# Kernel tuning notes

Hardware: AMD Instinct MI355X
Metric: run time of the kernel (lower is better)

The kernel has to match this reference:

```python
import jax, jax.numpy as jnp
import numpy as np

D_MODEL = 1024
D_STATE = 16
D_CONV = 4
EXPAND = 2
HEADDIM = 64
NGROUPS = 1
D_INNER = EXPAND * D_MODEL            # 2048
NHEADS = D_INNER // HEADDIM           # 32
CONV_DIM = D_INNER + 2 * NGROUPS * D_STATE   # 2080
D_IN_PROJ = 2 * D_INNER + 2 * NGROUPS * D_STATE + NHEADS  # 4160
EPS = 1e-5
BATCH, SEQLEN = 4, 2048


def setup_inputs() -> dict:
    key = jax.random.key(0)
    ks = jax.random.split(key, 8)
    x = jax.random.normal(ks[0], (BATCH, SEQLEN, D_MODEL), jnp.float32)
    W_in = jax.random.normal(ks[1], (D_MODEL, D_IN_PROJ), jnp.float32) * 0.02
    conv_w = jax.random.normal(ks[2], (CONV_DIM, D_CONV), jnp.float32) * 0.2
    conv_b = jnp.zeros((CONV_DIM,), jnp.float32)
    # dt_bias = inverse softplus of dt drawn in [1e-3, 1e-1] (mamba_ssm init)
    dt = jax.random.uniform(ks[3], (NHEADS,), jnp.float32, 0.001, 0.1)
    dt_bias = jnp.log(jnp.expm1(dt))
    A_log = jnp.log(jax.random.uniform(ks[4], (NHEADS,), jnp.float32, 1.0, 16.0))
    D_param = jnp.ones((NHEADS,), jnp.float32)
    norm_w = jnp.ones((D_INNER,), jnp.float32)
    W_out = jax.random.normal(ks[5], (D_INNER, D_MODEL), jnp.float32) * 0.02
    layer_scale = jnp.full((D_MODEL,), 1e-4, jnp.float32)
    return dict(x=x, W_in=W_in, conv_w=conv_w, conv_b=conv_b, dt_bias=dt_bias,
                A_log=A_log, D_param=D_param, norm_w=norm_w, W_out=W_out,
                layer_scale=layer_scale)


def _silu(v):
    return v * jax.nn.sigmoid(v)


def _mamba2(x, W_in, conv_w, conv_b, dt_bias, A_log, D_param, norm_w, W_out):
    b, l, _ = x.shape
    zxbcdt = x @ W_in                                  # (b, l, d_in_proj)
    z = zxbcdt[..., :D_INNER]                          # gate
    xBC = zxbcdt[..., D_INNER:D_INNER + CONV_DIM]
    dt = jax.nn.softplus(zxbcdt[..., D_INNER + CONV_DIM:] + dt_bias)  # (b, l, h)
    # causal depthwise conv1d (kernel D_CONV) + SiLU
    xp = jnp.pad(xBC, ((0, 0), (D_CONV - 1, 0), (0, 0)))
    conv = sum(xp[:, k:k + l, :] * conv_w[:, k] for k in range(D_CONV)) + conv_b
    xBC = _silu(conv)
    xs = xBC[..., :D_INNER].reshape(b, l, NHEADS, HEADDIM)  # (b, l, h, p)
    Bm = xBC[..., D_INNER:D_INNER + D_STATE]                # (b, l, n), ngroups=1
    Cm = xBC[..., D_INNER + D_STATE:]                       # (b, l, n)
    A = -jnp.exp(A_log)                                     # (h,)
    dA = jnp.exp(dt * A)                                    # (b, l, h)
    dtx = dt[..., None] * xs                                # (b, l, h, p)

    def step(h, inp):
        dA_t, dtx_t, B_t, C_t = inp
        # h: (b, h, p, n)
        h = h * dA_t[..., None, None] + dtx_t[..., None] * B_t[:, None, None, :]
        y = jnp.einsum('bhpn,bn->bhp', h, C_t)
        return h, y

    h0 = jnp.zeros((b, NHEADS, HEADDIM, D_STATE), x.dtype)
    _, ys = jax.lax.scan(step, h0, (dA.transpose(1, 0, 2), dtx.transpose(1, 0, 2, 3),
                                    Bm.transpose(1, 0, 2), Cm.transpose(1, 0, 2)))
    y = ys.transpose(1, 0, 2, 3) + D_param[None, None, :, None] * xs  # (b, l, h, p)
    y = y.reshape(b, l, D_INNER)
    # gated RMSNorm (norm_before_gate=False): gate first, then rmsnorm
    y = y * _silu(z)
    y = y * jax.lax.rsqrt(jnp.mean(y * y, axis=-1, keepdims=True) + EPS) * norm_w
    return y @ W_out


def reference(x, W_in, conv_w, conv_b, dt_bias, A_log, D_param, norm_w, W_out, layer_scale):
    # dropout is identity (eval / p=0)
    return x + _mamba2(x, W_in, conv_w, conv_b, dt_bias, A_log, D_param, norm_w, W_out) * layer_scale
```

## Files before the change

kernel.cpp:

```cpp
#include <hip/hip_runtime.h>
#include <hip/hip_bf16.h>

#define D_MODEL   1024
#define D_STATE   16
#define D_CONV    4
#define HEADDIM   64
#define NHEADS    32
#define D_INNER   2048
#define CONV_DIM  2080
#define D_IN_PROJ 4160
#define NPAD      4224
#define BATCH     4
#define SEQLEN    2048
#define MROWS     (BATCH*SEQLEN)
#define QCHUNK    64
#define NCHUNK    (SEQLEN/QCHUNK)
#define DT_COL    (2*D_INNER + 2*D_STATE)

#define WSCALE    16.f
#define YSCALE    64.f

__device__ __forceinline__ unsigned short f2b(float f) {
    union { float f; unsigned int u; } v; v.f = f;
    unsigned int r = (v.u + 0x7FFFu + ((v.u >> 16) & 1u)) >> 16;
    return (unsigned short)r;
}
__device__ __forceinline__ float b2f(unsigned short h) {
    union { unsigned int u; float f; } v; v.u = ((unsigned int)h) << 16;
    return v.f;
}
__device__ __forceinline__ unsigned char f2fp8(float f) {
    return (unsigned char)(__builtin_amdgcn_cvt_pk_fp8_f32(f, 0.f, 0, false) & 0xFF);
}

typedef __attribute__((ext_vector_type(8))) short bf16x8;
typedef __attribute__((ext_vector_type(4))) float f32x4;
typedef __attribute__((ext_vector_type(4))) int   i32x4;
typedef __attribute__((ext_vector_type(8))) int   i32x8;

__device__ __forceinline__ i32x8 cat8(i32x4 a, i32x4 b) {
    i32x8 r;
    r[0] = a[0]; r[1] = a[1]; r[2] = a[2]; r[3] = a[3];
    r[4] = b[0]; r[5] = b[1]; r[6] = b[2]; r[7] = b[3];
    return r;
}

__device__ __forceinline__ void async_copy16b(const unsigned char* g, unsigned char* l) {
    __builtin_amdgcn_global_load_lds(
        (const __attribute__((address_space(1))) void*)g,
        (__attribute__((address_space(3))) void*)l, 16, 0, 0);
}

__global__ __launch_bounds__(256)
void pre_kernel(const float* __restrict__ x, unsigned char* __restrict__ x_f8,
                const float* __restrict__ W_in, unsigned char* __restrict__ winT,
                const float* __restrict__ W_out, unsigned char* __restrict__ woutT,
                const float* __restrict__ norm_w) {
    __shared__ float tile[64][65];
    int bid = blockIdx.x;
    if (bid < 8192) {
        int i = (bid * 256 + threadIdx.x) * 4;
        float4 v = *(const float4*)&x[i];
        int p = __builtin_amdgcn_cvt_pk_fp8_f32(v.x, v.y, 0, false);
        p = __builtin_amdgcn_cvt_pk_fp8_f32(v.z, v.w, p, true);
        *(unsigned int*)&x_f8[i] = (unsigned int)p;
        return;
    }
    bid -= 8192;
    const float* W; unsigned char* WT; const float* kscale;
    int K, N, bx, by;
    if (bid < 1056) { W = W_in;  WT = winT;  kscale = nullptr; K = 1024; N = 4160; bx = bid % 66; by = bid / 66; }
    else { bid -= 1056; W = W_out; WT = woutT; kscale = norm_w; K = 2048; N = 1024; bx = bid % 16; by = bid / 16; }
    int n0 = bx * 64, k0 = by * 64;
    int tx = threadIdx.x & 63, ty = threadIdx.x >> 6;
    #pragma unroll
    for (int i = 0; i < 16; i++) {
        int r = ty * 16 + i;
        int n = n0 + tx;
        float v = (n < N) ? W[(size_t)(k0 + r) * N + n] : 0.f;
        tile[r][tx] = v;
    }
    __syncthreads();
    float ks = WSCALE * (kscale ? kscale[k0 + tx] : 1.f);
    #pragma unroll
    for (int i = 0; i < 16; i++) {
        int r = ty * 16 + i;
        WT[(size_t)(n0 + r) * K + k0 + tx] = f2fp8(tile[tx][r] * ks);
    }
}

template <int EPI, int NF>
__global__ __launch_bounds__(256)
void gemm_fp8(const unsigned char* __restrict__ A, const unsigned char* __restrict__ B,
              int K, int N, unsigned short* __restrict__ Cb,
              float* __restrict__ Cf, const float* __restrict__ xres,
              const float* __restrict__ ls, const float* __restrict__ ssq) {
    constexpr int BN = NF * 32;
    __shared__ unsigned char lds_a[128 * 128];
    __shared__ unsigned char lds_b[BN * 128];
    const int tid  = threadIdx.x;
    const int wave = tid >> 6;
    const int lane = tid & 63;
    const int bid = blockIdx.x;
    const int xcd = bid & 7, g = bid >> 3;
    const int bm = xcd * 8 + (g & 7);
    const int bn = g >> 3;
    const int wm = wave >> 1, wn = wave & 1;

    f32x4 acc[4][NF];
    #pragma unroll
    for (int i = 0; i < 4; i++)
        #pragma unroll
        for (int j = 0; j < NF; j++) acc[i][j] = (f32x4){0.f, 0.f, 0.f, 0.f};

    const int srow = lane >> 3;
    const int sseg = (lane & 7) ^ srow;
    const unsigned char* gA0 = A + (size_t)(bm * 128 + wave * 8 + srow) * K + sseg * 16;
    const unsigned char* gB0 = B + (size_t)(bn * BN  + wave * 8 + srow) * K + sseg * 16;
    const int ldsbase = wave * 8 * 128;

    const int lm = lane & 15, q = lane >> 4;

    for (int k0 = 0; k0 < K; k0 += 128) {
        #pragma unroll
        for (int j = 0; j < 4; j++)
            async_copy16b(gA0 + k0 + (size_t)(j * 32) * K, &lds_a[ldsbase + j * 32 * 128]);
        #pragma unroll
        for (int j = 0; j < NF; j++)
            async_copy16b(gB0 + k0 + (size_t)(j * 32) * K, &lds_b[ldsbase + j * 32 * 128]);
        __syncthreads();

        i32x8 af[4], bfr[NF];
        #pragma unroll
        for (int i = 0; i < 4; i++) {
            int r = wm * 64 + i * 16 + lm;
            int s0 = ((2 * q) ^ (r & 7)) * 16, s1 = ((2 * q + 1) ^ (r & 7)) * 16;
            af[i] = cat8(*(const i32x4*)&lds_a[r * 128 + s0],
                         *(const i32x4*)&lds_a[r * 128 + s1]);
        }
        #pragma unroll
        for (int j = 0; j < NF; j++) {
            int r = wn * (NF * 16) + j * 16 + lm;
            int s0 = ((2 * q) ^ (r & 7)) * 16, s1 = ((2 * q + 1) ^ (r & 7)) * 16;
            bfr[j] = cat8(*(const i32x4*)&lds_b[r * 128 + s0],
                          *(const i32x4*)&lds_b[r * 128 + s1]);
        }
        #pragma unroll
        for (int i = 0; i < 4; i++)
            #pragma unroll
            for (int j = 0; j < NF; j++)
                acc[i][j] = __builtin_amdgcn_mfma_scale_f32_16x16x128_f8f6f4(
                    af[i], bfr[j], acc[i][j], 0, 0,
                    0, 0x7F7F7F7F, 0, 0x7F7F7F7F);
        __syncthreads();
    }

    float* srs = (float*)lds_a;
    if constexpr (EPI == 1) {
        if (tid < 128) {
            const float4* p = (const float4*)&ssq[(size_t)(bm * 128 + tid) * NHEADS];
            float s = 0.f;
            #pragma unroll
            for (int i2 = 0; i2 < 8; i2++) {
                float4 v4 = p[i2];
                s += v4.x + v4.y + v4.z + v4.w;
            }
            srs[tid] = rsqrtf(s * (1.f / D_INNER) + 1e-5f);
        }
        __syncthreads();
    }

    const int row0 = bm * 128 + wm * 64;
    const int col0 = bn * BN + wn * (NF * 16);
    const int lq = (lane >> 4) * 4;
    #pragma unroll
    for (int i = 0; i < 4; i++) {
        #pragma unroll
        for (int j = 0; j < NF; j++) {
            #pragma unroll
            for (int r = 0; r < 4; r++) {
                int gr = row0 + i * 16 + lq + r;
                int gc = col0 + j * 16 + lm;
                float v = acc[i][j][r];
                if constexpr (EPI == 0) {
                    Cb[(size_t)gr * N + gc] = f2b(v * (1.f / WSCALE));
                } else {
                    size_t idx = (size_t)gr * 1024 + gc;
                    float rsv = srs[wm * 64 + i * 16 + lq + r];
                    Cf[idx] = xres[idx] + v * ls[gc] * rsv * (1.f / (WSCALE * YSCALE));
                }
            }
        }
    }
}

__global__ __launch_bounds__(256)
void ssd_hcomp(const unsigned short* __restrict__ zx, const float* __restrict__ dt_bias,
               const float* __restrict__ conv_w, const float* __restrict__ conv_b,
               const float* __restrict__ A_log,
               float* __restrict__ hbuf, float* __restrict__ pbuf,
               unsigned short* __restrict__ xTg, unsigned short* __restrict__ bcg,
               float* __restrict__ scA) {
    __shared__ unsigned short sXraw[67 * 64];
    __shared__ unsigned short sBCraw[67 * 32];
    __shared__ unsigned short sXT[64 * 72];
    __shared__ unsigned short sBC[64 * 32];
    __shared__ unsigned short sBwT[16 * 72];
    __shared__ float sdt[64], scd[64];

    const int blk = blockIdx.x;
    const int c  = blk & 31;
    const int h  = (blk >> 5) & 31;
    const int b  = blk >> 10;
    const int bh = blk >> 5;
    const int row0 = b * SEQLEN + c * QCHUNK;
    const int batch0 = b * SEQLEN;

    const int t    = threadIdx.x;
    const int w    = t >> 6;
    const int lane = t & 63;
    const int lm   = lane & 15;
    const int lq8  = (lane >> 4) * 8;
    const int lq4  = (lane >> 4) * 4;
    const float Ah = -__expf(A_log[h]);

    for (int i = t; i < 536; i += 256) {
        int r = i >> 3, seg = i & 7;
        int gr = row0 - 3 + r;
        int4 v = (gr >= batch0) ? *(const int4*)&zx[(size_t)gr * NPAD + D_INNER + h * 64 + seg * 8]
                                : (int4){0, 0, 0, 0};
        *(int4*)&sXraw[r * 64 + seg * 8] = v;
    }
    for (int i = t; i < 268; i += 256) {
        int r = i >> 2, seg = i & 3;
        int gr = row0 - 3 + r;
        int4 v = (gr >= batch0) ? *(const int4*)&zx[(size_t)gr * NPAD + 2 * D_INNER + seg * 8]
                                : (int4){0, 0, 0, 0};
        *(int4*)&sBCraw[r * 32 + seg * 8] = v;
    }
    if (t < 64) {
        float raw = b2f(zx[(size_t)(row0 + t) * NPAD + DT_COL + h]) + dt_bias[h];
        float dtv = (raw > 20.f) ? raw : log1pf(__expf(raw));
        float v = dtv;
        #pragma unroll
        for (int o = 1; o < 64; o <<= 1) {
            float u = __shfl_up(v, o, 64);
            if (t >= o) v += u;
        }
        sdt[t] = dtv;
        scd[t] = v;
        float sc = __expf(Ah * v);
        float* scrow = &scA[(size_t)(bh * NCHUNK + c) * 192];
        scrow[t] = dtv; scrow[64 + t] = v; scrow[128 + t] = sc;
        if (t == 63) pbuf[bh * NCHUNK + c] = sc;
    }
    __syncthreads();

    {
        const int p = t & 63, sblk = (t >> 6) * 16;
        const int ch = h * 64 + p;
        const float4 cw = *(const float4*)&conv_w[ch * 4];
        const float cb = conv_b[ch];
        float x0 = b2f(sXraw[(sblk + 0) * 64 + p]);
        float x1 = b2f(sXraw[(sblk + 1) * 64 + p]);
        float x2 = b2f(sXraw[(sblk + 2) * 64 + p]);
        #pragma unroll
        for (int i = 0; i < 16; i++) {
            float x3 = b2f(sXraw[(sblk + i + 3) * 64 + p]);
            float acc = cb + cw.x * x0 + cw.y * x1 + cw.z * x2 + cw.w * x3;
            float sv = acc / (1.f + __expf(-acc));
            sXT[p * 72 + sblk + i] = f2b(sv);
            x0 = x1; x1 = x2; x2 = x3;
        }
    }
    {
        const int ch32 = t & 31, s0 = (t >> 5) * 8;
        const int ch = D_INNER + ch32;
        const float4 cw = *(const float4*)&conv_w[ch * 4];
        const float cb = conv_b[ch];
        const float cdl = scd[63];
        float x0 = b2f(sBCraw[(s0 + 0) * 32 + ch32]);
        float x1 = b2f(sBCraw[(s0 + 1) * 32 + ch32]);
        float x2 = b2f(sBCraw[(s0 + 2) * 32 + ch32]);
        #pragma unroll
        for (int i = 0; i < 8; i++) {
            int s = s0 + i;
            float x3 = b2f(sBCraw[(s + 3) * 32 + ch32]);
            float acc = cb + cw.x * x0 + cw.y * x1 + cw.z * x2 + cw.w * x3;
            float sv = acc / (1.f + __expf(-acc));
            sBC[s * 32 + ch32] = f2b(sv);
            if (ch32 < 16) {
                float wgt = sdt[s] * __expf(Ah * (cdl - scd[s]));
                sBwT[ch32 * 72 + s] = f2b(sv * wgt);
            }
            x0 = x1; x1 = x2; x2 = x3;
        }
    }
    __syncthreads();

    f32x4 hacc = (f32x4){0.f, 0.f, 0.f, 0.f};
    #pragma unroll
    for (int ks = 0; ks < 2; ks++) {
        bf16x8 af = *(const bf16x8*)&sBwT[lm * 72 + ks * 32 + lq8];
        bf16x8 bf_ = *(const bf16x8*)&sXT[(w * 16 + lm) * 72 + ks * 32 + lq8];
        hacc = __builtin_amdgcn_mfma_f32_16x16x32_bf16(af, bf_, hacc, 0, 0, 0);
    }
    #pragma unroll
    for (int r = 0; r < 4; r++)
        hbuf[(size_t)(bh * NCHUNK + c) * 1024 + (lq4 + r) * 64 + (w * 16 + lm)] = hacc[r];

    #pragma unroll
    for (int it = 0; it < 2; it++) {
        int idx = t + it * 256;
        int p = idx >> 3, seg = idx & 7;
        *(int4*)&xTg[(size_t)(bh * 64 + p) * SEQLEN + c * 64 + seg * 8] =
            *(const int4*)&sXT[p * 72 + seg * 8];
    }
    if (h == 0) {
        int s = t >> 2, seg = t & 3;
        *(int4*)&bcg[(size_t)(b * SEQLEN + c * 64 + s) * 32 + seg * 8] =
            *(const int4*)&sBC[s * 32 + seg * 8];
    }
}

__global__ __launch_bounds__(1024)
void ssd_state_scan(float* __restrict__ hbuf, const float* __restrict__ pbuf) {
    int bh = blockIdx.x;
    int t = threadIdx.x;
    __shared__ float sP[NCHUNK];
    if (t < NCHUNK) sP[t] = pbuf[bh * NCHUNK + t];
    __syncthreads();
    size_t base = (size_t)bh * NCHUNK * 1024 + t;
    float v[NCHUNK];
    #pragma unroll
    for (int c = 0; c < NCHUNK; c++) v[c] = hbuf[base + (size_t)c * 1024];
    float carry = 0.f;
    #pragma unroll
    for (int c = 0; c < NCHUNK; c++) {
        float tmp = v[c];
        v[c] = carry;
        carry = tmp + sP[c] * carry;
    }
    #pragma unroll
    for (int c = 0; c < NCHUNK; c++) hbuf[base + (size_t)c * 1024] = v[c];
}

__global__ __launch_bounds__(256)
void ssd_yfused(const unsigned short* __restrict__ zx,
                const unsigned short* __restrict__ xTg, const unsigned short* __restrict__ bcg,
                const float* __restrict__ scA,
                const float* __restrict__ A_log, const float* __restrict__ D_param,
                const float* __restrict__ hbuf,
                unsigned char* __restrict__ y, float* __restrict__ ssq) {
    __shared__ unsigned short sXT[64 * 72];
    __shared__ unsigned short sM[64 * 72];
    __shared__ unsigned short sB[64 * 32];
    __shared__ unsigned short sC[64 * 32];
    __shared__ unsigned short sHT[64 * 40];
    __shared__ float sdt[64], scd[64], sSc[64];

    const int blk = blockIdx.x;
    const int c  = blk & 31;
    const int h  = (blk >> 5) & 31;
    const int b  = blk >> 10;
    const int bh = blk >> 5;
    const int row0 = b * SEQLEN + c * QCHUNK;

    const int t    = threadIdx.x;
    const int w    = t >> 6;
    const int lane = t & 63;
    const int lm   = lane & 15;
    const int lq8  = (lane >> 4) * 8;
    const int lq4  = (lane >> 4) * 4;
    const float Ah = -__expf(A_log[h]);

    unsigned short zreg[4][4];
    #pragma unroll
    for (int r = 0; r < 4; r++)
        #pragma unroll
        for (int pb = 0; pb < 4; pb++)
            zreg[r][pb] = zx[(size_t)(row0 + w * 16 + lq4 + r) * NPAD + h * 64 + pb * 16 + lm];

    #pragma unroll
    for (int it = 0; it < 2; it++) {
        int idx = t + it * 256;
        int p = idx >> 3, seg = idx & 7;
        *(int4*)&sXT[p * 72 + seg * 8] =
            *(const int4*)&xTg[(size_t)(bh * 64 + p) * SEQLEN + c * 64 + seg * 8];
    }
    {
        int s = t >> 2, seg = t & 3;
        int4 v = *(const int4*)&bcg[(size_t)(b * SEQLEN + c * 64 + s) * 32 + seg * 8];
        if (seg < 2) *(int4*)&sB[s * 32 + seg * 8] = v;
        else         *(int4*)&sC[s * 32 + (seg - 2) * 8] = v;
    }
    {
        size_t hb = (size_t)(bh * NCHUNK + c) * 1024 + (size_t)t * 4;
        float4 hv = *(const float4*)&hbuf[hb];
        int n = t >> 4;
        int p0 = (t * 4) & 63;
        sHT[(p0 + 0) * 40 + n] = f2b(hv.x);
        sHT[(p0 + 1) * 40 + n] = f2b(hv.y);
        sHT[(p0 + 2) * 40 + n] = f2b(hv.z);
        sHT[(p0 + 3) * 40 + n] = f2b(hv.w);
    }
    if (t < 64) {
        *(int4*)&sB[t * 32 + 16] = (int4){0, 0, 0, 0};
        *(int4*)&sB[t * 32 + 24] = (int4){0, 0, 0, 0};
        *(int4*)&sC[t * 32 + 16] = (int4){0, 0, 0, 0};
        *(int4*)&sC[t * 32 + 24] = (int4){0, 0, 0, 0};
        *(int4*)&sHT[t * 40 + 16] = (int4){0, 0, 0, 0};
        *(int4*)&sHT[t * 40 + 24] = (int4){0, 0, 0, 0};
    }
    if (t < 192) {
        float v = scA[(size_t)(bh * NCHUNK + c) * 192 + t];
        if (t < 64) sdt[t] = v;
        else if (t < 128) scd[t - 64] = v;
        else sSc[t - 128] = v;
    }
    __syncthreads();

    f32x4 sacc[4];
    {
        bf16x8 cfrag = *(const bf16x8*)&sC[(w * 16 + lm) * 32 + lq8];
        #pragma unroll
        for (int sb = 0; sb < 4; sb++) {
            if (sb <= w) {
                bf16x8 bfrag = *(const bf16x8*)&sB[(sb * 16 + lm) * 32 + lq8];
                sacc[sb] = __builtin_amdgcn_mfma_f32_16x16x32_bf16(
                    cfrag, bfrag, (f32x4){0.f, 0.f, 0.f, 0.f}, 0, 0, 0);
            }
        }
    }
    const float Dh = D_param[h];
    #pragma unroll
    for (int sb = 0; sb < 4; sb++) {
        int sp = sb * 16 + lm;
        if (sb > w) {
            #pragma unroll
            for (int r = 0; r < 4; r++) sM[(w * 16 + lq4 + r) * 72 + sp] = 0;
        } else {
            float dts = sdt[sp], cds = scd[sp];
            #pragma unroll
            for (int r = 0; r < 4; r++) {
                int tp = w * 16 + lq4 + r;
                float m = 0.f;
                if (sb < w || sp <= tp) {
                    m = sacc[sb][r] * dts * __expf(Ah * (scd[tp] - cds));
                    if (sp == tp) m += Dh;
                }
                sM[tp * 72 + sp] = f2b(m);
            }
        }
    }

    f32x4 yacc[4];
    #pragma unroll
    for (int pb = 0; pb < 4; pb++) yacc[pb] = (f32x4){0.f, 0.f, 0.f, 0.f};
    #pragma unroll
    for (int ks = 0; ks < 2; ks++) {
        if (ks == 1 && w < 2) continue;
        bf16x8 af = *(const bf16x8*)&sM[(w * 16 + lm) * 72 + ks * 32 + lq8];
        #pragma unroll
        for (int pb = 0; pb < 4; pb++) {
            bf16x8 bf_ = *(const bf16x8*)&sXT[(pb * 16 + lm) * 72 + ks * 32 + lq8];
            yacc[pb] = __builtin_amdgcn_mfma_f32_16x16x32_bf16(af, bf_, yacc[pb], 0, 0, 0);
        }
    }
    f32x4 acc2[4];
    {
        bf16x8 cf2 = *(const bf16x8*)&sC[(w * 16 + lm) * 32 + lq8];
        #pragma unroll
        for (int pb = 0; pb < 4; pb++) {
            bf16x8 hf = *(const bf16x8*)&sHT[(pb * 16 + lm) * 40 + lq8];
            acc2[pb] = __builtin_amdgcn_mfma_f32_16x16x32_bf16(
                cf2, hf, (f32x4){0.f, 0.f, 0.f, 0.f}, 0, 0, 0);
        }
    }

    #pragma unroll
    for (int r = 0; r < 4; r++) {
        const int tp = w * 16 + lq4 + r;
        const size_t yrow = (size_t)(row0 + tp) * D_INNER + h * 64;
        float ssr = 0.f;
        #pragma unroll
        for (int pb = 0; pb < 4; pb++) {
            int pp = pb * 16 + lm;
            float val = yacc[pb][r] + sSc[tp] * acc2[pb][r];
            float zv = b2f(zreg[r][pb]);
            float yg = val * (zv / (1.f + __expf(-zv)));
            ssr += yg * yg;
            y[yrow + pp] = f2fp8(yg * YSCALE);
        }
        ssr += __shfl_xor(ssr, 1, 16);
        ssr += __shfl_xor(ssr, 2, 16);
        ssr += __shfl_xor(ssr, 4, 16);
        ssr += __shfl_xor(ssr, 8, 16);
        if (lm == 0)
            ssq[(size_t)(row0 + tp) * NHEADS + h] = ssr;
    }
}

extern "C" void kernel_launch(void* const* d_in, const int* in_sizes, int n_in,
                              void* d_out, int out_size, void* d_ws, size_t ws_size,
                              hipStream_t stream) {
    const float* x        = (const float*)d_in[0];
    const float* W_in     = (const float*)d_in[1];
    const float* conv_w   = (const float*)d_in[2];
    const float* conv_b   = (const float*)d_in[3];
    const float* dt_bias  = (const float*)d_in[4];
    const float* A_log    = (const float*)d_in[5];
    const float* D_param  = (const float*)d_in[6];
    const float* norm_w   = (const float*)d_in[7];
    const float* W_out    = (const float*)d_in[8];
    const float* ls       = (const float*)d_in[9];
    float* out = (float*)d_out;

    char* ws = (char*)d_ws;
    size_t off = 0;
    unsigned char*  x_f8  = (unsigned char*)(ws + off);  off += (size_t)MROWS * D_MODEL;
    unsigned char*  winT  = (unsigned char*)(ws + off);  off += (size_t)NPAD * D_MODEL;
    unsigned char*  woutT = (unsigned char*)(ws + off);  off += (size_t)D_MODEL * D_INNER;
    unsigned short* zx    = (unsigned short*)(ws + off); off += (size_t)MROWS * NPAD * 2;
    float*          pbuf  = (float*)(ws + off);          off += (size_t)BATCH * NHEADS * NCHUNK * 4;
    unsigned char*  yb    = (unsigned char*)(ws + off);  off += (size_t)MROWS * D_INNER;
    float*          ssq   = (float*)(ws + off);          off += (size_t)MROWS * NHEADS * 4;
    float*          hbuf  = (float*)(ws + off);          off += (size_t)BATCH * NHEADS * NCHUNK * 1024 * 4;
    unsigned short* xTg   = (unsigned short*)(ws + off); off += (size_t)MROWS * D_INNER * 2;
    unsigned short* bcg   = (unsigned short*)(ws + off); off += (size_t)MROWS * 32 * 2;
    float*          scA   = (float*)(ws + off);          off += (size_t)BATCH * NHEADS * NCHUNK * 192 * 4;

    pre_kernel<<<8192 + 1568, 256, 0, stream>>>(x, x_f8, W_in, winT, W_out, woutT, norm_w);
    gemm_fp8<0, 4><<<(NPAD / 128) * 64, 256, 0, stream>>>(
        x_f8, winT, D_MODEL, NPAD, zx, nullptr, nullptr, nullptr, nullptr);
    ssd_hcomp<<<BATCH * NHEADS * NCHUNK, 256, 0, stream>>>(
        zx, dt_bias, conv_w, conv_b, A_log, hbuf, pbuf, xTg, bcg, scA);
    ssd_state_scan<<<BATCH * NHEADS, 1024, 0, stream>>>(hbuf, pbuf);
    ssd_yfused<<<BATCH * NHEADS * NCHUNK, 256, 0, stream>>>(
        zx, xTg, bcg, scA, A_log, D_param, hbuf, yb, ssq);
    gemm_fp8<1, 2><<<(D_MODEL / 64) * 64, 256, 0, stream>>>(
        yb, woutT, D_INNER, D_MODEL, nullptr, out, x, ls, ssq);
}
```

Measured before the change: 269.6 us.

## Recompute conv+SiLU in y kernel and store chunk states as bf16

Stops writing the conv-activated x (transposed, bf16) to global memory in the state kernel. The y kernel instead reloads the raw x slice from the projection output and recomputes the causal conv and SiLU into shared memory, reusing the mask buffer as staging. Chunk states are also stored in bf16 instead of fp32, which halves state traffic through the scan. The cost is extra compute and a sync in the y kernel, plus bf16 rounding of the states before the inter-chunk scan, which may reduce accuracy.

```diff
diff --git a/kernel.cpp b/kernel.cpp
--- a/kernel.cpp
+++ b/kernel.cpp
@@ -198,9 +198,8 @@
 void ssd_hcomp(const unsigned short* __restrict__ zx, const float* __restrict__ dt_bias,
                const float* __restrict__ conv_w, const float* __restrict__ conv_b,
                const float* __restrict__ A_log,
-               float* __restrict__ hbuf, float* __restrict__ pbuf,
-               unsigned short* __restrict__ xTg, unsigned short* __restrict__ bcg,
-               float* __restrict__ scA) {
+               unsigned short* __restrict__ hbuf, float* __restrict__ pbuf,
+               unsigned short* __restrict__ bcg, float* __restrict__ scA) {
     __shared__ unsigned short sXraw[67 * 64];
     __shared__ unsigned short sBCraw[67 * 32];
     __shared__ unsigned short sXT[64 * 72];
@@ -307,15 +306,8 @@
     }
     #pragma unroll
     for (int r = 0; r < 4; r++)
-        hbuf[(size_t)(bh * NCHUNK + c) * 1024 + (lq4 + r) * 64 + (w * 16 + lm)] = hacc[r];
-
-    #pragma unroll
-    for (int it = 0; it < 2; it++) {
-        int idx = t + it * 256;
-        int p = idx >> 3, seg = idx & 7;
-        *(int4*)&xTg[(size_t)(bh * 64 + p) * SEQLEN + c * 64 + seg * 8] =
-            *(const int4*)&sXT[p * 72 + seg * 8];
-    }
+        hbuf[(size_t)(bh * NCHUNK + c) * 1024 + (lq4 + r) * 64 + (w * 16 + lm)] = f2b(hacc[r]);
+
     if (h == 0) {
         int s = t >> 2, seg = t & 3;
         *(int4*)&bcg[(size_t)(b * SEQLEN + c * 64 + s) * 32 + seg * 8] =
@@ -324,7 +316,7 @@
 }
 
 __global__ __launch_bounds__(1024)
-void ssd_state_scan(float* __restrict__ hbuf, const float* __restrict__ pbuf) {
+void ssd_state_scan(unsigned short* __restrict__ hbuf, const float* __restrict__ pbuf) {
     int bh = blockIdx.x;
     int t = threadIdx.x;
     __shared__ float sP[NCHUNK];
@@ -333,7 +325,7 @@
     size_t base = (size_t)bh * NCHUNK * 1024 + t;
     float v[NCHUNK];
     #pragma unroll
-    for (int c = 0; c < NCHUNK; c++) v[c] = hbuf[base + (size_t)c * 1024];
+    for (int c = 0; c < NCHUNK; c++) v[c] = b2f(hbuf[base + (size_t)c * 1024]);
     float carry = 0.f;
     #pragma unroll
     for (int c = 0; c < NCHUNK; c++) {
@@ -342,22 +334,25 @@
         carry = tmp + sP[c] * carry;
     }
     #pragma unroll
-    for (int c = 0; c < NCHUNK; c++) hbuf[base + (size_t)c * 1024] = v[c];
+    for (int c = 0; c < NCHUNK; c++) hbuf[base + (size_t)c * 1024] = f2b(v[c]);
 }
 
 __global__ __launch_bounds__(256)
 void ssd_yfused(const unsigned short* __restrict__ zx,
-                const unsigned short* __restrict__ xTg, const unsigned short* __restrict__ bcg,
+                const float* __restrict__ conv_w, const float* __restrict__ conv_b,
+                const unsigned short* __restrict__ bcg,
                 const float* __restrict__ scA,
                 const float* __restrict__ A_log, const float* __restrict__ D_param,
-                const float* __restrict__ hbuf,
+                const unsigned short* __restrict__ hbuf,
                 unsigned char* __restrict__ y, float* __restrict__ ssq) {
     __shared__ unsigned short sXT[64 * 72];
-    __shared__ unsigned short sM[64 * 72];
+    __shared__ unsigned short sMX[64 * 72];
     __shared__ unsigned short sB[64 * 32];
     __shared__ unsigned short sC[64 * 32];
     __shared__ unsigned short sHT[64 * 40];
     __shared__ float sdt[64], scd[64], sSc[64];
+    unsigned short* sXraw = sMX;
+    unsigned short* sM    = sMX;
 
     const int blk = blockIdx.x;
     const int c  = blk & 31;
@@ -365,6 +360,7 @@
     const int b  = blk >> 10;
     const int bh = blk >> 5;
     const int row0 = b * SEQLEN + c * QCHUNK;
+    const int batch0 = b * SEQLEN;
 
     const int t    = threadIdx.x;
     const int w    = t >> 6;
@@ -381,12 +377,12 @@
         for (int pb = 0; pb < 4; pb++)
             zreg[r][pb] = zx[(size_t)(row0 + w * 16 + lq4 + r) * NPAD + h * 64 + pb * 16 + lm];
 
-    #pragma unroll
-    for (int it = 0; it < 2; it++) {
-        int idx = t + it * 256;
-        int p = idx >> 3, seg = idx & 7;
-        *(int4*)&sXT[p * 72 + seg * 8] =
-            *(const int4*)&xTg[(size_t)(bh * 64 + p) * SEQLEN + c * 64 + seg * 8];
+    for (int i = t; i < 536; i += 256) {
+        int r = i >> 3, seg = i & 7;
+        int gr = row0 - 3 + r;
+        int4 v = (gr >= batch0) ? *(const int4*)&zx[(size_t)gr * NPAD + D_INNER + h * 64 + seg * 8]
+                                : (int4){0, 0, 0, 0};
+        *(int4*)&sXraw[r * 64 + seg * 8] = v;
     }
     {
         int s = t >> 2, seg = t & 3;
@@ -396,13 +392,13 @@
     }
     {
         size_t hb = (size_t)(bh * NCHUNK + c) * 1024 + (size_t)t * 4;
-        float4 hv = *(const float4*)&hbuf[hb];
+        const unsigned short* hp = &hbuf[hb];
         int n = t >> 4;
         int p0 = (t * 4) & 63;
-        sHT[(p0 + 0) * 40 + n] = f2b(hv.x);
-        sHT[(p0 + 1) * 40 + n] = f2b(hv.y);
-        sHT[(p0 + 2) * 40 + n] = f2b(hv.z);
-        sHT[(p0 + 3) * 40 + n] = f2b(hv.w);
+        sHT[(p0 + 0) * 40 + n] = hp[0];
+        sHT[(p0 + 1) * 40 + n] = hp[1];
+        sHT[(p0 + 2) * 40 + n] = hp[2];
+        sHT[(p0 + 3) * 40 + n] = hp[3];
     }
     if (t < 64) {
         *(int4*)&sB[t * 32 + 16] = (int4){0, 0, 0, 0};
@@ -432,6 +428,25 @@
             }
         }
     }
+    {
+        const int p = t & 63, sblk = (t >> 6) * 16;
+        const int ch = h * 64 + p;
+        const float4 cw = *(const float4*)&conv_w[ch * 4];
+        const float cb = conv_b[ch];
+        float x0 = b2f(sXraw[(sblk + 0) * 64 + p]);
+        float x1 = b2f(sXraw[(sblk + 1) * 64 + p]);
+        float x2 = b2f(sXraw[(sblk + 2) * 64 + p]);
+        #pragma unroll
+        for (int i = 0; i < 16; i++) {
+            float x3 = b2f(sXraw[(sblk + i + 3) * 64 + p]);
+            float acc = cb + cw.x * x0 + cw.y * x1 + cw.z * x2 + cw.w * x3;
+            float sv = acc / (1.f + __expf(-acc));
+            sXT[p * 72 + sblk + i] = f2b(sv);
+            x0 = x1; x1 = x2; x2 = x3;
+        }
+    }
+    __syncthreads();
+
     const float Dh = D_param[h];
     #pragma unroll
     for (int sb = 0; sb < 4; sb++) {
@@ -525,8 +540,7 @@
     float*          pbuf  = (float*)(ws + off);          off += (size_t)BATCH * NHEADS * NCHUNK * 4;
     unsigned char*  yb    = (unsigned char*)(ws + off);  off += (size_t)MROWS * D_INNER;
     float*          ssq   = (float*)(ws + off);          off += (size_t)MROWS * NHEADS * 4;
-    float*          hbuf  = (float*)(ws + off);          off += (size_t)BATCH * NHEADS * NCHUNK * 1024 * 4;
-    unsigned short* xTg   = (unsigned short*)(ws + off); off += (size_t)MROWS * D_INNER * 2;
+    unsigned short* hbuf  = (unsigned short*)(ws + off); off += (size_t)BATCH * NHEADS * NCHUNK * 1024 * 2;
     unsigned short* bcg   = (unsigned short*)(ws + off); off += (size_t)MROWS * 32 * 2;
     float*          scA   = (float*)(ws + off);          off += (size_t)BATCH * NHEADS * NCHUNK * 192 * 4;
 
@@ -534,10 +548,10 @@
     gemm_fp8<0, 4><<<(NPAD / 128) * 64, 256, 0, stream>>>(
         x_f8, winT, D_MODEL, NPAD, zx, nullptr, nullptr, nullptr, nullptr);
     ssd_hcomp<<<BATCH * NHEADS * NCHUNK, 256, 0, stream>>>(
-        zx, dt_bias, conv_w, conv_b, A_log, hbuf, pbuf, xTg, bcg, scA);
+        zx, dt_bias, conv_w, conv_b, A_log, hbuf, pbuf, bcg, scA);
     ssd_state_scan<<<BATCH * NHEADS, 1024, 0, stream>>>(hbuf, pbuf);
     ssd_yfused<<<BATCH * NHEADS * NCHUNK, 256, 0, stream>>>(
-        zx, xTg, bcg, scA, A_log, D_param, hbuf, yb, ssq);
+        zx, conv_w, conv_b, bcg, scA, A_log, D_param, hbuf, yb, ssq);
     gemm_fp8<1, 2><<<(D_MODEL / 64) * 64, 256, 0, stream>>>(
         yb, woutT, D_INNER, D_MODEL, nullptr, out, x, ls, ssq);
 }
```

Result: no change. 268.1 us (-0.5%).
